# Kernel optimization log

Hardware: AMD Instinct MI355X
Metric: run time of the kernel (lower is better)

Reference implementation:

```python
import jax, jax.numpy as jnp
import numpy as np

B, N, M, Wlen = 4, 20000, 64, 8


def setup_inputs() -> dict:
    key = jax.random.key(0)
    k1, k2, k3, k4 = jax.random.split(key, 4)
    a0 = jax.random.uniform(k1, (B, N), dtype=jnp.float32)
    W = 0.01 * jax.random.normal(k2, (M, M), dtype=jnp.float32)
    X1 = jax.random.randint(k3, (M, N, Wlen, 2), 0, N, dtype=jnp.int64)
    X2 = jax.random.randint(k4, (M, N, Wlen, 2), 0, N, dtype=jnp.int64)
    return {"a0": a0, "W": W, "X1": X1, "X2": X2, "T": 2}


def f_clause_stack(a, X):
    # a: [B,n], X: [m,n,w,2] -> [B,m,n]
    y1 = a[:, X[..., 0]]  # [B,m,n,w] gather
    y2 = a[:, X[..., 1]]
    return jnp.max(y1 * y2, axis=3)


def predicate_forward(a, W, X1, X2, temperature=1.0):
    F1 = f_clause_stack(a, X1)  # [B,m1,n]
    F2 = f_clause_stack(a, X2)  # [B,m2,n]
    pi = jax.nn.softmax((W / temperature).reshape(-1)).reshape(W.shape)  # [m1,m2]
    pi1 = pi.sum(axis=1)  # [m1]
    pi2 = pi.sum(axis=0)  # [m2]
    Eu = jnp.einsum('j,bjn->bn', pi1, F1)
    Ev = jnp.einsum('k,bkn->bn', pi2, F2)
    Mt = jnp.einsum('jk,bkn->bjn', pi, F2)
    Euv = jnp.sum(F1 * Mt, axis=1)
    return Eu + Ev - Euv  # [B,n]


def reference(a0, W, X1, X2, T):
    a = a0
    for _ in range(T):  # T is a small static int
        derived = predicate_forward(a, W, X1, X2)
        # single intensional predicate -> stack/max over predicates is identity
        a = 1.0 - (1.0 - a) * (1.0 - derived)
    return a
```

## Files before the change

kernel.cpp:

```cpp
#include <hip/hip_runtime.h>

#define NN 20000
#define COLS 40
#define CPAD 41

typedef _Float16 f16x2 __attribute__((ext_vector_type(2)));
typedef unsigned short u16x2 __attribute__((ext_vector_type(2)));

union U32H2 { unsigned int u; f16x2 h; };
union U32S2 { unsigned int u; u16x2 s; };

__device__ __forceinline__ f16x2 bc_h2(unsigned int u) { U32H2 x; x.u = u; return x.h; }
__device__ __forceinline__ unsigned int dup_h(float v) {
    _Float16 h = (_Float16)v;
    unsigned short b = __builtin_bit_cast(unsigned short, h);
    return ((unsigned int)b << 16) | b;
}
__device__ __forceinline__ unsigned int pkrtz_u32(float a, float b) {
    return __builtin_bit_cast(unsigned int, __builtin_amdgcn_cvt_pkrtz(a, b));
}

template <int CTRL>
__device__ __forceinline__ unsigned int pkmax_dpp(unsigned int v) {
    unsigned int d = (unsigned int)__builtin_amdgcn_update_dpp(
        0, (int)v, CTRL, 0xF, 0xF, true);
    U32S2 a, b; a.u = v; b.u = d;
    a.s = __builtin_elementwise_max(a.s, b.s);
    return a.u;
}
__device__ __forceinline__ unsigned int octmax_u16x2(unsigned int v) {
    v = pkmax_dpp<0xB1>(v);
    v = pkmax_dpp<0x4E>(v);
    v = pkmax_dpp<0x141>(v);
    return v;
}

__global__ __launch_bounds__(1024) void prep_kernel(const float* __restrict__ W,
                                                    unsigned int* __restrict__ pi_pk,
                                                    unsigned int* __restrict__ pi_t_pk,
                                                    unsigned int* __restrict__ pi1_pk,
                                                    unsigned int* __restrict__ pi2_pk) {
    __shared__ float red[1024];
    __shared__ float piL[4096];
    int t = threadIdx.x;
    float4 wv = ((const float4*)W)[t];
    float m = fmaxf(fmaxf(wv.x, wv.y), fmaxf(wv.z, wv.w));
    red[t] = m; __syncthreads();
    for (int s = 512; s > 0; s >>= 1) {
        if (t < s) red[t] = fmaxf(red[t], red[t + s]);
        __syncthreads();
    }
    m = red[0];
    __syncthreads();
    float e0 = expf(wv.x - m), e1 = expf(wv.y - m);
    float e2 = expf(wv.z - m), e3 = expf(wv.w - m);
    red[t] = e0 + e1 + e2 + e3;
    __syncthreads();
    for (int s = 512; s > 0; s >>= 1) {
        if (t < s) red[t] += red[t + s];
        __syncthreads();
    }
    float inv = 1.0f / red[0];
    float p[4] = { e0 * inv, e1 * inv, e2 * inv, e3 * inv };
#pragma unroll
    for (int i = 0; i < 4; i++) {
        int f = t * 4 + i;
        piL[f] = p[i];
        unsigned int d = dup_h(p[i]);
        pi_pk[f] = d;
        pi_t_pk[(f & 63) * 64 + (f >> 6)] = d;
    }
    __syncthreads();
    if (t < 64) {
        float s = 0.f;
        for (int k = 0; k < 64; k++) s += piL[t * 64 + k];
        pi1_pk[t] = dup_h(s);
    } else if (t < 128) {
        int k = t - 64;
        float s = 0.f;
        for (int j = 0; j < 64; j++) s += piL[j * 64 + k];
        pi2_pk[k] = dup_h(s);
    }
}

__global__ __launch_bounds__(1024) void pack_kernel(const float* __restrict__ a0,
                                                    unsigned int* __restrict__ T0) {
    int i = blockIdx.x * 1024 + threadIdx.x;
    if (i < NN) {
        unsigned int b0 = __float2uint_rn(__saturatef(a0[i]) * 255.0f);
        unsigned int b1 = __float2uint_rn(__saturatef(a0[NN + i]) * 255.0f);
        unsigned int b2 = __float2uint_rn(__saturatef(a0[2 * NN + i]) * 255.0f);
        unsigned int b3 = __float2uint_rn(__saturatef(a0[3 * NN + i]) * 255.0f);
        T0[i] = b0 | (b1 << 8) | (b2 << 16) | (b3 << 24);
    }
}

__device__ __forceinline__ void phase1(
    const unsigned int* __restrict__ tab,
    unsigned int (* __restrict__ Ftb)[2][CPAD],
    const int* __restrict__ X1, const int* __restrict__ X2,
    int nb, int cn, int widu, int ni, int w) {
    const float sc = 1.0f / 65025.0f;
    int loff[5];
#pragma unroll
    for (int oc = 0; oc < 5; ++oc) {
        int n = nb + oc * 8 + ni;
        int nc = n < NN ? n : NN - 1;
        loff[oc] = nc * 64 + w * 8;
    }
    int2 qb[2][5];
#pragma unroll
    for (int d = 0; d < 2; ++d) {
        const int row = widu + 16 * d, k = row & 63;
        const char* Xb = (const char*)((row >> 6) ? X2 : X1) + (unsigned)(k * NN) * 64u;
#pragma unroll
        for (int oc = 0; oc < 5; ++oc) qb[d][oc] = *(const int2*)(Xb + loff[oc]);
    }
#pragma unroll
    for (int rr = 0; rr < 8; ++rr) {
        const int cur = rr & 1;
        unsigned int ga[5], gb[5];
#pragma unroll
        for (int oc = 0; oc < 5; ++oc) {
            ga[oc] = tab[qb[cur][oc].x];
            gb[oc] = tab[qb[cur][oc].y];
        }
        if (rr < 6) {
            const int row2 = widu + 16 * (rr + 2), k2 = row2 & 63;
            const char* Xb = (const char*)((row2 >> 6) ? X2 : X1)
                           + (unsigned)(k2 * NN) * 64u;
#pragma unroll
            for (int oc = 0; oc < 5; ++oc) qb[cur][oc] = *(const int2*)(Xb + loff[oc]);
        }
        const int row = widu + 16 * rr;
#pragma unroll
        for (int oc = 0; oc < 5; ++oc) {
            unsigned int ea = ga[oc] & 0x00FF00FFu;
            unsigned int oa = (ga[oc] >> 8) & 0x00FF00FFu;
            unsigned int eb = gb[oc] & 0x00FF00FFu;
            unsigned int ob = (gb[oc] >> 8) & 0x00FF00FFu;
            U32S2 pe, po, xb;
            pe.u = ea; xb.u = eb; pe.s = pe.s * xb.s;
            po.u = oa; xb.u = ob; po.s = po.s * xb.s;
            unsigned int peu = octmax_u16x2(pe.u);
            unsigned int pou = octmax_u16x2(po.u);
            int col = oc * 8 + ni;
            if (w == 0 && col < cn) {
                float f0 = (float)(peu & 0xFFFFu) * sc;
                float f1 = (float)(pou & 0xFFFFu) * sc;
                float f2 = (float)(peu >> 16) * sc;
                float f3 = (float)(pou >> 16) * sc;
                Ftb[row][0][col] = pkrtz_u32(f0, f1);
                Ftb[row][1][col] = pkrtz_u32(f2, f3);
            }
        }
    }
}

__device__ __forceinline__ float2 phase2(
    const unsigned int (* __restrict__ Ftb)[2][CPAD],
    const unsigned int* __restrict__ pi_t_pk,
    const unsigned int* __restrict__ pi1_pk,
    const unsigned int* __restrict__ pi2_pk,
    int qu, int bp, int n_l) {
    f16x2 zero = {(_Float16)0, (_Float16)0};
    f16x2 f1v[8];
    f16x2 eu = zero;
#pragma unroll
    for (int jj = 0; jj < 8; ++jj) {
        f1v[jj] = bc_h2(Ftb[qu * 8 + jj][bp][n_l]);
        eu += bc_h2(pi1_pk[qu * 8 + jj]) * f1v[jj];
    }
    f16x2 euv = zero, ev = zero;
#pragma unroll 8
    for (int k = 0; k < 64; ++k) {
        f16x2 f2 = bc_h2(Ftb[64 + k][bp][n_l]);
        const uint4* pt = (const uint4*)(pi_t_pk + k * 64 + qu * 8);
        uint4 w0 = pt[0], w1 = pt[1];
        f16x2 ts = bc_h2(w0.x) * f1v[0] + bc_h2(w0.y) * f1v[1] +
                   bc_h2(w0.z) * f1v[2] + bc_h2(w0.w) * f1v[3] +
                   bc_h2(w1.x) * f1v[4] + bc_h2(w1.y) * f1v[5] +
                   bc_h2(w1.z) * f1v[6] + bc_h2(w1.w) * f1v[7];
        euv += f2 * ts;
        if (qu == 0) ev += bc_h2(pi2_pk[k]) * f2;
    }
    float p0 = (float)eu[0] - (float)euv[0];
    float p1 = (float)eu[1] - (float)euv[1];
    if (qu == 0) { p0 += (float)ev[0]; p1 += (float)ev[1]; }
    return make_float2(p0, p1);
}

template <int ITER>
__global__ __launch_bounds__(1024, 4) void fused_iter(
    const unsigned int* __restrict__ Tsrc,
    const int* __restrict__ X1, const int* __restrict__ X2,
    const unsigned int* __restrict__ pi_t_pk,
    const unsigned int* __restrict__ pi1_pk,
    const unsigned int* __restrict__ pi2_pk,
    const float* __restrict__ a0,
    unsigned int* __restrict__ Tdst, float* __restrict__ outP) {
    __shared__ unsigned int tab[NN];
    __shared__ unsigned int Ft[128][2][CPAD];
    __shared__ float redp[8][64][4];

    const int t = threadIdx.x;
    for (int i = t; i < NN; i += 1024) tab[i] = Tsrc[i];

    const int bid = (int)blockIdx.x;
    const int bstart = bid < 32 ? bid * 79 : 32 * 79 + (bid - 32) * 78;
    const int bcnt = bid < 32 ? 79 : 78;
    const int c0 = (bcnt + 1) >> 1;

    const int wid = t >> 6, lane = t & 63, ni = lane >> 3, w = lane & 7;
    const int q = t >> 7, bp = (t >> 6) & 1, n_l = t & 63;
    const int widu = __builtin_amdgcn_readfirstlane(wid);
    const int qu = __builtin_amdgcn_readfirstlane(q);

    __syncthreads();

    for (int ch = 0; ch < 2; ++ch) {
        const int nb = bstart + (ch ? c0 : 0);
        const int cn = ch ? (bcnt - c0) : c0;

        phase1(tab, Ft, X1, X2, nb, cn, widu, ni, w);
        __syncthreads();

        if (n_l < cn) {
            float2 pp = phase2(Ft, pi_t_pk, pi1_pk, pi2_pk, qu, bp, n_l);
            *(float2*)&redp[q][n_l][bp * 2] = pp;
        }
        __syncthreads();

        if (t < cn) {
            int gn = nb + t;
            float d0 = 0.f, d1 = 0.f, d2 = 0.f, d3 = 0.f;
#pragma unroll
            for (int q8 = 0; q8 < 8; ++q8) {
                d0 += redp[q8][t][0];
                d1 += redp[q8][t][1];
                d2 += redp[q8][t][2];
                d3 += redp[q8][t][3];
            }
            float ap0, ap1, ap2, ap3;
            if (ITER == 1) {
                ap0 = a0[gn]; ap1 = a0[NN + gn];
                ap2 = a0[2 * NN + gn]; ap3 = a0[3 * NN + gn];
            } else {
                unsigned int tv = tab[gn];
                ap0 = (float)(tv & 255u) * (1.0f / 255.0f);
                ap1 = (float)((tv >> 8) & 255u) * (1.0f / 255.0f);
                ap2 = (float)((tv >> 16) & 255u) * (1.0f / 255.0f);
                ap3 = (float)(tv >> 24) * (1.0f / 255.0f);
            }
            float an0 = 1.0f - (1.0f - ap0) * (1.0f - d0);
            float an1 = 1.0f - (1.0f - ap1) * (1.0f - d1);
            float an2 = 1.0f - (1.0f - ap2) * (1.0f - d2);
            float an3 = 1.0f - (1.0f - ap3) * (1.0f - d3);
            if (ITER == 1) {
                unsigned int b0 = __float2uint_rn(__saturatef(an0) * 255.0f);
                unsigned int b1 = __float2uint_rn(__saturatef(an1) * 255.0f);
                unsigned int b2 = __float2uint_rn(__saturatef(an2) * 255.0f);
                unsigned int b3 = __float2uint_rn(__saturatef(an3) * 255.0f);
                Tdst[gn] = b0 | (b1 << 8) | (b2 << 16) | (b3 << 24);
            } else {
                outP[gn] = an0;
                outP[NN + gn] = an1;
                outP[2 * NN + gn] = an2;
                outP[3 * NN + gn] = an3;
            }
        }
    }
}

extern "C" void kernel_launch(void* const* d_in, const int* in_sizes, int n_in,
                              void* d_out, int out_size, void* d_ws, size_t ws_size,
                              hipStream_t stream) {
    const float* a0 = (const float*)d_in[0];
    const float* W = (const float*)d_in[1];
    const int* X1 = (const int*)d_in[2];
    const int* X2 = (const int*)d_in[3];
    float* out = (float*)d_out;

    if (ws_size < (size_t)193280) return;
    unsigned int* pi_pk  = (unsigned int*)d_ws;
    unsigned int* pi_t   = (unsigned int*)((char*)d_ws + 16384);
    unsigned int* pi1_pk = (unsigned int*)((char*)d_ws + 32768);
    unsigned int* pi2_pk = (unsigned int*)((char*)d_ws + 33024);
    unsigned int* T0     = (unsigned int*)((char*)d_ws + 33280);
    unsigned int* T1     = (unsigned int*)((char*)d_ws + 113280);

    prep_kernel<<<1, 1024, 0, stream>>>(W, pi_pk, pi_t, pi1_pk, pi2_pk);
    pack_kernel<<<20, 1024, 0, stream>>>(a0, T0);
    fused_iter<1><<<256, 1024, 0, stream>>>(T0, X1, X2, pi_t, pi1_pk, pi2_pk,
                                            a0, T1, nullptr);
    fused_iter<2><<<256, 1024, 0, stream>>>(T1, X1, X2, pi_t, pi1_pk, pi2_pk,
                                            nullptr, nullptr, out);
}
```

Baseline: 250.0 us.

## Assign each thread a full clause window and reduce max in registers

Phase 1 is remapped so each thread owns one clause row and five consecutive columns. It loads the whole 8-pair index window (64 bytes) as four int4 vector loads and reduces the max in registers, instead of spreading the window across 8 lanes and combining with DPP cross-lane max. This removes the DPP shuffles and the w==0 store predicate, and it lets every lane do useful gather work. The trade-off is higher register pressure and a per-thread strided global access pattern: 64-byte chunks spaced by column, which may coalesce less well than the previous layout where 8 lanes read contiguous int2 values.

Measured after the change: 255.4 us. +2.2%, slower.

```diff
diff --git a/kernel.cpp b/kernel.cpp
--- a/kernel.cpp
+++ b/kernel.cpp
@@ -19,20 +19,8 @@
 __device__ __forceinline__ unsigned int pkrtz_u32(float a, float b) {
     return __builtin_bit_cast(unsigned int, __builtin_amdgcn_cvt_pkrtz(a, b));
 }
-
-template <int CTRL>
-__device__ __forceinline__ unsigned int pkmax_dpp(unsigned int v) {
-    unsigned int d = (unsigned int)__builtin_amdgcn_update_dpp(
-        0, (int)v, CTRL, 0xF, 0xF, true);
-    U32S2 a, b; a.u = v; b.u = d;
-    a.s = __builtin_elementwise_max(a.s, b.s);
-    return a.u;
-}
-__device__ __forceinline__ unsigned int octmax_u16x2(unsigned int v) {
-    v = pkmax_dpp<0xB1>(v);
-    v = pkmax_dpp<0x4E>(v);
-    v = pkmax_dpp<0x141>(v);
-    return v;
+__device__ __forceinline__ u16x2 pkmax2(u16x2 a, u16x2 b) {
+    return __builtin_elementwise_max(a, b);
 }
 
 __global__ __launch_bounds__(1024) void prep_kernel(const float* __restrict__ W,
@@ -98,62 +86,64 @@
 __device__ __forceinline__ void phase1(
     const unsigned int* __restrict__ tab,
     unsigned int (* __restrict__ Ftb)[2][CPAD],
-    const int* __restrict__ X1, const int* __restrict__ X2,
-    int nb, int cn, int widu, int ni, int w) {
+    const int* __restrict__ Xp,
+    int rowk,
+    int row,
+    int col0,
+    int nb, int cn) {
     const float sc = 1.0f / 65025.0f;
-    int loff[5];
-#pragma unroll
-    for (int oc = 0; oc < 5; ++oc) {
-        int n = nb + oc * 8 + ni;
-        int nc = n < NN ? n : NN - 1;
-        loff[oc] = nc * 64 + w * 8;
-    }
-    int2 qb[2][5];
-#pragma unroll
-    for (int d = 0; d < 2; ++d) {
-        const int row = widu + 16 * d, k = row & 63;
-        const char* Xb = (const char*)((row >> 6) ? X2 : X1) + (unsigned)(k * NN) * 64u;
-#pragma unroll
-        for (int oc = 0; oc < 5; ++oc) qb[d][oc] = *(const int2*)(Xb + loff[oc]);
-    }
-#pragma unroll
-    for (int rr = 0; rr < 8; ++rr) {
-        const int cur = rr & 1;
-        unsigned int ga[5], gb[5];
-#pragma unroll
-        for (int oc = 0; oc < 5; ++oc) {
-            ga[oc] = tab[qb[cur][oc].x];
-            gb[oc] = tab[qb[cur][oc].y];
-        }
-        if (rr < 6) {
-            const int row2 = widu + 16 * (rr + 2), k2 = row2 & 63;
-            const char* Xb = (const char*)((row2 >> 6) ? X2 : X1)
-                           + (unsigned)(k2 * NN) * 64u;
-#pragma unroll
-            for (int oc = 0; oc < 5; ++oc) qb[cur][oc] = *(const int2*)(Xb + loff[oc]);
-        }
-        const int row = widu + 16 * rr;
-#pragma unroll
-        for (int oc = 0; oc < 5; ++oc) {
-            unsigned int ea = ga[oc] & 0x00FF00FFu;
-            unsigned int oa = (ga[oc] >> 8) & 0x00FF00FFu;
-            unsigned int eb = gb[oc] & 0x00FF00FFu;
-            unsigned int ob = (gb[oc] >> 8) & 0x00FF00FFu;
-            U32S2 pe, po, xb;
-            pe.u = ea; xb.u = eb; pe.s = pe.s * xb.s;
-            po.u = oa; xb.u = ob; po.s = po.s * xb.s;
-            unsigned int peu = octmax_u16x2(pe.u);
-            unsigned int pou = octmax_u16x2(po.u);
-            int col = oc * 8 + ni;
-            if (w == 0 && col < cn) {
-                float f0 = (float)(peu & 0xFFFFu) * sc;
-                float f1 = (float)(pou & 0xFFFFu) * sc;
-                float f2 = (float)(peu >> 16) * sc;
-                float f3 = (float)(pou >> 16) * sc;
-                Ftb[row][0][col] = pkrtz_u32(f0, f1);
-                Ftb[row][1][col] = pkrtz_u32(f2, f3);
-            }
-        }
+    const char* Xb = (const char*)Xp;
+    unsigned int roff = (unsigned int)rowk * (unsigned int)(NN * 64);
+    int4 xq[4];
+    {
+        int c = 0;
+        int n = nb + (c < cn ? col0 + c : 0);
+        const int4* p = (const int4*)(Xb + roff + (unsigned int)n * 64u);
+        xq[0] = p[0]; xq[1] = p[1]; xq[2] = p[2]; xq[3] = p[3];
+    }
+#pragma unroll
+    for (int tk = 0; tk < 5; ++tk) {
+        int4 nx[4];
+        if (tk < 4) {
+            int c = tk + 1;
+            int n = nb + (col0 + c < cn ? col0 + c : 0);
+            const int4* p = (const int4*)(Xb + roff + (unsigned int)n * 64u);
+            nx[0] = p[0]; nx[1] = p[1]; nx[2] = p[2]; nx[3] = p[3];
+        }
+        unsigned int ga[8], gb[8];
+#pragma unroll
+        for (int i = 0; i < 4; ++i) {
+            ga[2 * i]     = tab[xq[i].x];
+            gb[2 * i]     = tab[xq[i].y];
+            ga[2 * i + 1] = tab[xq[i].z];
+            gb[2 * i + 1] = tab[xq[i].w];
+        }
+        u16x2 pe[8], po[8];
+#pragma unroll
+        for (int i = 0; i < 8; ++i) {
+            U32S2 a, b;
+            a.u = ga[i] & 0x00FF00FFu; b.u = gb[i] & 0x00FF00FFu;
+            pe[i] = a.s * b.s;
+            a.u = (ga[i] >> 8) & 0x00FF00FFu; b.u = (gb[i] >> 8) & 0x00FF00FFu;
+            po[i] = a.s * b.s;
+        }
+        u16x2 e0 = pkmax2(pkmax2(pe[0], pe[1]), pkmax2(pe[2], pe[3]));
+        u16x2 e1 = pkmax2(pkmax2(pe[4], pe[5]), pkmax2(pe[6], pe[7]));
+        u16x2 o0 = pkmax2(pkmax2(po[0], po[1]), pkmax2(po[2], po[3]));
+        u16x2 o1 = pkmax2(pkmax2(po[4], po[5]), pkmax2(po[6], po[7]));
+        U32S2 peu, pou;
+        peu.s = pkmax2(e0, e1);
+        pou.s = pkmax2(o0, o1);
+        int col = col0 + tk;
+        if (col < cn) {
+            float f0 = (float)(peu.u & 0xFFFFu) * sc;
+            float f1 = (float)(pou.u & 0xFFFFu) * sc;
+            float f2 = (float)(peu.u >> 16) * sc;
+            float f3 = (float)(pou.u >> 16) * sc;
+            Ftb[row][0][col] = pkrtz_u32(f0, f1);
+            Ftb[row][1][col] = pkrtz_u32(f2, f3);
+        }
+        xq[0] = nx[0]; xq[1] = nx[1]; xq[2] = nx[2]; xq[3] = nx[3];
     }
 }
 
@@ -211,9 +201,10 @@
     const int bcnt = bid < 32 ? 79 : 78;
     const int c0 = (bcnt + 1) >> 1;
 
-    const int wid = t >> 6, lane = t & 63, ni = lane >> 3, w = lane & 7;
+    const int row = t >> 3, rowk = row & 63, col0 = (t & 7) * 5;
+    const int tsel = __builtin_amdgcn_readfirstlane(t >> 9);
+    const int* Xp = tsel ? X2 : X1;
     const int q = t >> 7, bp = (t >> 6) & 1, n_l = t & 63;
-    const int widu = __builtin_amdgcn_readfirstlane(wid);
     const int qu = __builtin_amdgcn_readfirstlane(q);
 
     __syncthreads();
@@ -222,7 +213,7 @@
         const int nb = bstart + (ch ? c0 : 0);
         const int cn = ch ? (bcnt - c0) : c0;
 
-        phase1(tab, Ft, X1, X2, nb, cn, widu, ni, w);
+        phase1(tab, Ft, Xp, rowk, row, col0, nb, cn);
         __syncthreads();
 
         if (n_l < cn) {
```

## Split batch pairs across blocks with 16-bit packed tables to halve LDS use

Applied to the files above, without the earlier changes.

Each block now handles two of the four batch rows, using a 16-bit per-node table and a grid of 2x256 blocks. The LDS footprint drops (tab 40KB instead of 80KB, Ft halved), and launch bounds are raised to 8 blocks per CU to increase occupancy. The cost is that index gathers from X1/X2 are repeated twice, once per batch pair, doubling global index traffic. Phase 2 also splits into 16 groups of four rows instead of 8 groups of eight.

Result: slower. 271.6 us (+8.7%).

```diff
diff --git a/kernel.cpp b/kernel.cpp
--- a/kernel.cpp
+++ b/kernel.cpp
@@ -1,7 +1,6 @@
 #include <hip/hip_runtime.h>
 
 #define NN 20000
-#define COLS 40
 #define CPAD 41
 
 typedef _Float16 f16x2 __attribute__((ext_vector_type(2)));
@@ -18,6 +17,9 @@
 }
 __device__ __forceinline__ unsigned int pkrtz_u32(float a, float b) {
     return __builtin_bit_cast(unsigned int, __builtin_amdgcn_cvt_pkrtz(a, b));
+}
+__device__ __forceinline__ unsigned int spread8(unsigned int g) {
+    return __builtin_amdgcn_perm(0u, g, 0x0C010C00u);
 }
 
 template <int CTRL>
@@ -84,20 +86,21 @@
 }
 
 __global__ __launch_bounds__(1024) void pack_kernel(const float* __restrict__ a0,
-                                                    unsigned int* __restrict__ T0) {
+                                                    unsigned short* __restrict__ T0) {
     int i = blockIdx.x * 1024 + threadIdx.x;
     if (i < NN) {
         unsigned int b0 = __float2uint_rn(__saturatef(a0[i]) * 255.0f);
         unsigned int b1 = __float2uint_rn(__saturatef(a0[NN + i]) * 255.0f);
         unsigned int b2 = __float2uint_rn(__saturatef(a0[2 * NN + i]) * 255.0f);
         unsigned int b3 = __float2uint_rn(__saturatef(a0[3 * NN + i]) * 255.0f);
-        T0[i] = b0 | (b1 << 8) | (b2 << 16) | (b3 << 24);
+        T0[i] = (unsigned short)(b0 | (b1 << 8));
+        T0[NN + i] = (unsigned short)(b2 | (b3 << 8));
     }
 }
 
 __device__ __forceinline__ void phase1(
-    const unsigned int* __restrict__ tab,
-    unsigned int (* __restrict__ Ftb)[2][CPAD],
+    const unsigned short* __restrict__ tab,
+    unsigned int (* __restrict__ Ftb)[CPAD],
     const int* __restrict__ X1, const int* __restrict__ X2,
     int nb, int cn, int widu, int ni, int w) {
     const float sc = 1.0f / 65025.0f;
@@ -135,86 +138,78 @@
         const int row = widu + 16 * rr;
 #pragma unroll
         for (int oc = 0; oc < 5; ++oc) {
-            unsigned int ea = ga[oc] & 0x00FF00FFu;
-            unsigned int oa = (ga[oc] >> 8) & 0x00FF00FFu;
-            unsigned int eb = gb[oc] & 0x00FF00FFu;
-            unsigned int ob = (gb[oc] >> 8) & 0x00FF00FFu;
-            U32S2 pe, po, xb;
-            pe.u = ea; xb.u = eb; pe.s = pe.s * xb.s;
-            po.u = oa; xb.u = ob; po.s = po.s * xb.s;
-            unsigned int peu = octmax_u16x2(pe.u);
-            unsigned int pou = octmax_u16x2(po.u);
+            U32S2 a, b;
+            a.u = spread8(ga[oc]);
+            b.u = spread8(gb[oc]);
+            a.s = a.s * b.s;
+            unsigned int peu = octmax_u16x2(a.u);
             int col = oc * 8 + ni;
             if (w == 0 && col < cn) {
                 float f0 = (float)(peu & 0xFFFFu) * sc;
-                float f1 = (float)(pou & 0xFFFFu) * sc;
-                float f2 = (float)(peu >> 16) * sc;
-                float f3 = (float)(pou >> 16) * sc;
-                Ftb[row][0][col] = pkrtz_u32(f0, f1);
-                Ftb[row][1][col] = pkrtz_u32(f2, f3);
+                float f1 = (float)(peu >> 16) * sc;
+                Ftb[row][col] = pkrtz_u32(f0, f1);
             }
         }
     }
 }
 
 __device__ __forceinline__ float2 phase2(
-    const unsigned int (* __restrict__ Ftb)[2][CPAD],
+    const unsigned int (* __restrict__ Ftb)[CPAD],
     const unsigned int* __restrict__ pi_t_pk,
     const unsigned int* __restrict__ pi1_pk,
     const unsigned int* __restrict__ pi2_pk,
-    int qu, int bp, int n_l) {
+    int gu, int n_l) {
     f16x2 zero = {(_Float16)0, (_Float16)0};
-    f16x2 f1v[8];
+    f16x2 f1v[4];
     f16x2 eu = zero;
 #pragma unroll
-    for (int jj = 0; jj < 8; ++jj) {
-        f1v[jj] = bc_h2(Ftb[qu * 8 + jj][bp][n_l]);
-        eu += bc_h2(pi1_pk[qu * 8 + jj]) * f1v[jj];
+    for (int ji = 0; ji < 4; ++ji) {
+        f1v[ji] = bc_h2(Ftb[gu * 4 + ji][n_l]);
+        eu += bc_h2(pi1_pk[gu * 4 + ji]) * f1v[ji];
     }
     f16x2 euv = zero, ev = zero;
 #pragma unroll 8
     for (int k = 0; k < 64; ++k) {
-        f16x2 f2 = bc_h2(Ftb[64 + k][bp][n_l]);
-        const uint4* pt = (const uint4*)(pi_t_pk + k * 64 + qu * 8);
-        uint4 w0 = pt[0], w1 = pt[1];
-        f16x2 ts = bc_h2(w0.x) * f1v[0] + bc_h2(w0.y) * f1v[1] +
-                   bc_h2(w0.z) * f1v[2] + bc_h2(w0.w) * f1v[3] +
-                   bc_h2(w1.x) * f1v[4] + bc_h2(w1.y) * f1v[5] +
-                   bc_h2(w1.z) * f1v[6] + bc_h2(w1.w) * f1v[7];
+        f16x2 f2 = bc_h2(Ftb[64 + k][n_l]);
+        uint4 wv = *(const uint4*)(pi_t_pk + k * 64 + gu * 4);
+        f16x2 ts = bc_h2(wv.x) * f1v[0] + bc_h2(wv.y) * f1v[1] +
+                   bc_h2(wv.z) * f1v[2] + bc_h2(wv.w) * f1v[3];
         euv += f2 * ts;
-        if (qu == 0) ev += bc_h2(pi2_pk[k]) * f2;
+        if (gu == 0) ev += bc_h2(pi2_pk[k]) * f2;
     }
     float p0 = (float)eu[0] - (float)euv[0];
     float p1 = (float)eu[1] - (float)euv[1];
-    if (qu == 0) { p0 += (float)ev[0]; p1 += (float)ev[1]; }
+    if (gu == 0) { p0 += (float)ev[0]; p1 += (float)ev[1]; }
     return make_float2(p0, p1);
 }
 
 template <int ITER>
-__global__ __launch_bounds__(1024, 4) void fused_iter(
-    const unsigned int* __restrict__ Tsrc,
+__global__ __launch_bounds__(1024, 8) void fused_iter(
+    const unsigned short* __restrict__ Tsrc,
     const int* __restrict__ X1, const int* __restrict__ X2,
     const unsigned int* __restrict__ pi_t_pk,
     const unsigned int* __restrict__ pi1_pk,
     const unsigned int* __restrict__ pi2_pk,
     const float* __restrict__ a0,
-    unsigned int* __restrict__ Tdst, float* __restrict__ outP) {
-    __shared__ unsigned int tab[NN];
-    __shared__ unsigned int Ft[128][2][CPAD];
-    __shared__ float redp[8][64][4];
+    unsigned short* __restrict__ Tdst, float* __restrict__ outP) {
+    __shared__ unsigned short tab[NN];
+    __shared__ unsigned int Ft[128][CPAD];
+    __shared__ float redp[16][64][2];
 
     const int t = threadIdx.x;
-    for (int i = t; i < NN; i += 1024) tab[i] = Tsrc[i];
-
-    const int bid = (int)blockIdx.x;
+    const int p = (int)blockIdx.x;
+    const unsigned short* Tp = Tsrc + p * NN;
+    for (int i = t; i < NN; i += 1024) tab[i] = Tp[i];
+
+    const int bid = (int)blockIdx.y;
     const int bstart = bid < 32 ? bid * 79 : 32 * 79 + (bid - 32) * 78;
     const int bcnt = bid < 32 ? 79 : 78;
     const int c0 = (bcnt + 1) >> 1;
 
     const int wid = t >> 6, lane = t & 63, ni = lane >> 3, w = lane & 7;
-    const int q = t >> 7, bp = (t >> 6) & 1, n_l = t & 63;
+    const int g = t >> 6, n_l = t & 63;
     const int widu = __builtin_amdgcn_readfirstlane(wid);
-    const int qu = __builtin_amdgcn_readfirstlane(q);
+    const int gu = widu;
 
     __syncthreads();
 
@@ -226,47 +221,37 @@
         __syncthreads();
 
         if (n_l < cn) {
-            float2 pp = phase2(Ft, pi_t_pk, pi1_pk, pi2_pk, qu, bp, n_l);
-            *(float2*)&redp[q][n_l][bp * 2] = pp;
+            float2 pp = phase2(Ft, pi_t_pk, pi1_pk, pi2_pk, gu, n_l);
+            *(float2*)&redp[g][n_l][0] = pp;
         }
         __syncthreads();
 
         if (t < cn) {
             int gn = nb + t;
-            float d0 = 0.f, d1 = 0.f, d2 = 0.f, d3 = 0.f;
-#pragma unroll
-            for (int q8 = 0; q8 < 8; ++q8) {
-                d0 += redp[q8][t][0];
-                d1 += redp[q8][t][1];
-                d2 += redp[q8][t][2];
-                d3 += redp[q8][t][3];
-            }
-            float ap0, ap1, ap2, ap3;
+            float d0 = 0.f, d1 = 0.f;
+#pragma unroll
+            for (int g16 = 0; g16 < 16; ++g16) {
+                d0 += redp[g16][t][0];
+                d1 += redp[g16][t][1];
+            }
+            float ap0, ap1;
             if (ITER == 1) {
-                ap0 = a0[gn]; ap1 = a0[NN + gn];
-                ap2 = a0[2 * NN + gn]; ap3 = a0[3 * NN + gn];
+                ap0 = a0[(size_t)(2 * p) * NN + gn];
+                ap1 = a0[(size_t)(2 * p + 1) * NN + gn];
             } else {
                 unsigned int tv = tab[gn];
                 ap0 = (float)(tv & 255u) * (1.0f / 255.0f);
-                ap1 = (float)((tv >> 8) & 255u) * (1.0f / 255.0f);
-                ap2 = (float)((tv >> 16) & 255u) * (1.0f / 255.0f);
-                ap3 = (float)(tv >> 24) * (1.0f / 255.0f);
+                ap1 = (float)(tv >> 8) * (1.0f / 255.0f);
             }
             float an0 = 1.0f - (1.0f - ap0) * (1.0f - d0);
             float an1 = 1.0f - (1.0f - ap1) * (1.0f - d1);
-            float an2 = 1.0f - (1.0f - ap2) * (1.0f - d2);
-            float an3 = 1.0f - (1.0f - ap3) * (1.0f - d3);
             if (ITER == 1) {
                 unsigned int b0 = __float2uint_rn(__saturatef(an0) * 255.0f);
                 unsigned int b1 = __float2uint_rn(__saturatef(an1) * 255.0f);
-                unsigned int b2 = __float2uint_rn(__saturatef(an2) * 255.0f);
-                unsigned int b3 = __float2uint_rn(__saturatef(an3) * 255.0f);
-                Tdst[gn] = b0 | (b1 << 8) | (b2 << 16) | (b3 << 24);
+                Tdst[p * NN + gn] = (unsigned short)(b0 | (b1 << 8));
             } else {
-                outP[gn] = an0;
-                outP[NN + gn] = an1;
-                outP[2 * NN + gn] = an2;
-                outP[3 * NN + gn] = an3;
+                outP[(size_t)(2 * p) * NN + gn] = an0;
+                outP[(size_t)(2 * p + 1) * NN + gn] = an1;
             }
         }
     }
@@ -286,13 +271,13 @@
     unsigned int* pi_t   = (unsigned int*)((char*)d_ws + 16384);
     unsigned int* pi1_pk = (unsigned int*)((char*)d_ws + 32768);
     unsigned int* pi2_pk = (unsigned int*)((char*)d_ws + 33024);
-    unsigned int* T0     = (unsigned int*)((char*)d_ws + 33280);
-    unsigned int* T1     = (unsigned int*)((char*)d_ws + 113280);
+    unsigned short* T0   = (unsigned short*)((char*)d_ws + 33280);
+    unsigned short* T1   = (unsigned short*)((char*)d_ws + 113280);
 
     prep_kernel<<<1, 1024, 0, stream>>>(W, pi_pk, pi_t, pi1_pk, pi2_pk);
     pack_kernel<<<20, 1024, 0, stream>>>(a0, T0);
-    fused_iter<1><<<256, 1024, 0, stream>>>(T0, X1, X2, pi_t, pi1_pk, pi2_pk,
-                                            a0, T1, nullptr);
-    fused_iter<2><<<256, 1024, 0, stream>>>(T1, X1, X2, pi_t, pi1_pk, pi2_pk,
-                                            nullptr, nullptr, out);
-}
+    fused_iter<1><<<dim3(2, 256), 1024, 0, stream>>>(T0, X1, X2, pi_t, pi1_pk,
+                                                     pi2_pk, a0, T1, nullptr);
+    fused_iter<2><<<dim3(2, 256), 1024, 0, stream>>>(T1, X1, X2, pi_t, pi1_pk,
+                                                     pi2_pk, nullptr, nullptr, out);
+}
```
